# Kernel tuning notes

Hardware: AMD Instinct MI355X
Metric: run time of the kernel (lower is better)

## Reference

```python
import jax, jax.numpy as jnp
import numpy as np
from math import sqrt

N = 400000
MUL0, MUL1 = 64, 32            # multiplicities of 0e and 1o in irreps_in1 / irreps_out
DIM_IN1 = MUL0 + 3 * MUL1      # 160 = e3nn layout [64x0e | 32x1o]

# UnnormalisedFullyConnectedTensorProduct path coefficients:
# path_weight = mul1*mul2*n_paths_to_out, irrep_normalization='component',
# path_normalization='path' => coeff = sqrt(ir_out.dim / (mul1*mul2*n_paths_to_out)).
# Each output irrep (0e and 1o) receives exactly 2 paths here.
C_SS0 = sqrt(1.0 / (MUL0 * 1 * 2))   # 0e x 0e -> 0e
C_VV0 = sqrt(1.0 / (MUL1 * 1 * 2))   # 1o x 1o -> 0e
C_SV1 = sqrt(3.0 / (MUL0 * 1 * 2))   # 0e x 1o -> 1o
C_VS1 = sqrt(3.0 / (MUL1 * 1 * 2))   # 1o x 0e -> 1o
INV_SQRT3 = 1.0 / sqrt(3.0)          # real-basis wigner_3j values for the l=1 paths


def setup_inputs() -> dict:
    key = jax.random.key(0)
    ks = jax.random.split(key, 7)
    return {
        "x1": jax.random.normal(ks[0], (N, DIM_IN1), jnp.float32),
        "x2": jax.random.normal(ks[1], (N, 4), jnp.float32),   # 1x0e + 1x1o attribute
        # uvw weights, one [mul1, mul2, mul_out] block per CG path
        "W_ss0": jax.random.normal(ks[2], (MUL0, 1, MUL0), jnp.float32) * 0.05,
        "W_vv0": jax.random.normal(ks[3], (MUL1, 1, MUL0), jnp.float32) * 0.05,
        "W_sv1": jax.random.normal(ks[4], (MUL0, 1, MUL1), jnp.float32) * 0.05,
        "W_vs1": jax.random.normal(ks[5], (MUL1, 1, MUL1), jnp.float32) * 0.05,
        # bias only for the scalar (0e) output slice
        "bias0": jax.random.normal(ks[6], (MUL0,), jnp.float32) * 0.05,
    }


def reference(x1, x2, W_ss0, W_vv0, W_sv1, W_vs1, bias0):
    # split e3nn-layout inputs into irrep blocks
    s1 = x1[:, :MUL0]                      # [N, 64]     0e block
    v1 = x1[:, MUL0:].reshape(-1, MUL1, 3) # [N, 32, 3]  1o block (mul-major)
    s2 = x2[:, :1]                         # [N, 1]
    v2 = x2[:, 1:].reshape(-1, 1, 3)       # [N, 1, 3]

    # scalar output: 0e x 0e -> 0e  (w3j = [[[1]]])
    out0 = C_SS0 * jnp.einsum('uvw,bu,bv->bw', W_ss0, s1, s2)
    # scalar output: 1o x 1o -> 0e  (w3j[i,j,0] = delta_ij / sqrt(3))
    out0 = out0 + (C_VV0 * INV_SQRT3) * jnp.einsum('uvw,bui,bvi->bw', W_vv0, v1, v2)
    # slice-wise bias add on l=0 channels
    out0 = out0 + bias0

    # vector output: 0e x 1o -> 1o  (w3j[0,j,k] = delta_jk / sqrt(3))
    out1 = (C_SV1 * INV_SQRT3) * jnp.einsum('uvw,bu,bvk->bwk', W_sv1, s1, v2)
    # vector output: 1o x 0e -> 1o  (w3j[i,0,k] = delta_ik / sqrt(3))
    out1 = out1 + (C_VS1 * INV_SQRT3) * jnp.einsum('uvw,bui,bv->bwi', W_vs1, v1, s2)

    return jnp.concatenate([out0, out1.reshape(-1, MUL1 * 3)], axis=-1)  # [N, 160]
```

## Files before the change

kernel.cpp:

```cpp
#include <hip/hip_runtime.h>

typedef __bf16 bf16x8 __attribute__((ext_vector_type(8)));
typedef float floatx4 __attribute__((ext_vector_type(4)));

static constexpr int ROW_IN  = 160;
static constexpr int ROW_OUT = 160;

static constexpr float C_SS0_F    = 0.08838834764831845f;
static constexpr float C_VV0_I3_F = 0.07216878364870323f;
static constexpr float C_SV1_I3_F = 0.08838834764831845f;
static constexpr float C_VS1_I3_F = 0.125f;

__device__ __forceinline__ floatx4 mfma16(bf16x8 a, bf16x8 b, floatx4 c) {
    return __builtin_amdgcn_mfma_f32_16x16x32_bf16(a, b, c, 0, 0, 0);
}

__global__ __launch_bounds__(256, 2)
void o3tp_kernel(const float* __restrict__ x1, const float* __restrict__ x2,
                 const float* __restrict__ Wss0, const float* __restrict__ Wvv0,
                 const float* __restrict__ Wsv1, const float* __restrict__ Wvs1,
                 const float* __restrict__ bias0, float* __restrict__ out, int n)
{
    const int lane = threadIdx.x & 63;
    const int m = lane & 15;
    const int q = lane >> 4;

    bf16x8 Wss[2][4];
    bf16x8 Wvv[4];
    bf16x8 Wsv[2][2];
    bf16x8 Wvs[2];
#pragma unroll
    for (int kt = 0; kt < 2; ++kt)
#pragma unroll
        for (int ct = 0; ct < 4; ++ct)
#pragma unroll
            for (int j = 0; j < 8; ++j)
                Wss[kt][ct][j] = (__bf16)Wss0[(kt*32 + q*8 + j)*64 + ct*16 + m];
#pragma unroll
    for (int ct = 0; ct < 4; ++ct)
#pragma unroll
        for (int j = 0; j < 8; ++j)
            Wvv[ct][j] = (__bf16)Wvv0[(q*8 + j)*64 + ct*16 + m];
#pragma unroll
    for (int kt = 0; kt < 2; ++kt)
#pragma unroll
        for (int ct = 0; ct < 2; ++ct)
#pragma unroll
            for (int j = 0; j < 8; ++j)
                Wsv[kt][ct][j] = (__bf16)(Wsv1[(kt*32 + q*8 + j)*32 + ct*16 + m] * C_SV1_I3_F);
#pragma unroll
    for (int ct = 0; ct < 2; ++ct)
#pragma unroll
        for (int j = 0; j < 8; ++j)
            Wvs[ct][j] = (__bf16)Wvs1[(q*8 + j)*32 + ct*16 + m];

    floatx4 bias_v[4];
#pragma unroll
    for (int ct = 0; ct < 4; ++ct)
        bias_v[ct] = *(const floatx4*)(bias0 + ct*16 + q*4);

    const floatx4 zero = {0.f, 0.f, 0.f, 0.f};

    const int n_tiles = n >> 4;
    const int wid     = blockIdx.x * (blockDim.x >> 6) + (threadIdx.x >> 6);
    const int n_waves = gridDim.x * (blockDim.x >> 6);

    float4 rs[4];
    float4 rc[6];
    float4 rx2;

    auto LOAD = [&](int tile) {
        const float* __restrict__ src = x1 + (size_t)(tile*16 + m) * ROW_IN;
        rs[0] = *(const float4*)(src + q*8);
        rs[1] = *(const float4*)(src + q*8 + 4);
        rs[2] = *(const float4*)(src + 32 + q*8);
        rs[3] = *(const float4*)(src + 32 + q*8 + 4);
#pragma unroll
        for (int t = 0; t < 6; ++t)
            rc[t] = *(const float4*)(src + 64 + q*24 + t*4);
        rx2 = *(const float4*)(x2 + (size_t)(tile*16 + m) * 4);
    };

    int tile = wid;
    if (tile < n_tiles) LOAD(tile);

    for (; tile < n_tiles; ) {
        bf16x8 a_s[2], a_ss[2];
        const float sscale = rx2.x * C_SS0_F;
#pragma unroll
        for (int kt = 0; kt < 2; ++kt) {
            const float vv[8] = {rs[2*kt].x, rs[2*kt].y, rs[2*kt].z, rs[2*kt].w,
                                 rs[2*kt+1].x, rs[2*kt+1].y, rs[2*kt+1].z, rs[2*kt+1].w};
#pragma unroll
            for (int j = 0; j < 8; ++j) {
                a_s[kt][j]  = (__bf16)vv[j];
                a_ss[kt][j] = (__bf16)(vv[j] * sscale);
            }
        }
        float c[24];
#pragma unroll
        for (int t = 0; t < 6; ++t) {
            c[t*4+0] = rc[t].x; c[t*4+1] = rc[t].y; c[t*4+2] = rc[t].z; c[t*4+3] = rc[t].w;
        }
        bf16x8 a_d, a_v0, a_v1, a_v2;
        const float gscale = rx2.x * C_VS1_I3_F;
        const float xy = rx2.y, xz = rx2.z, xw = rx2.w;
#pragma unroll
        for (int j = 0; j < 8; ++j) {
            const float d = (c[3*j+0]*xy + c[3*j+1]*xz + c[3*j+2]*xw) * C_VV0_I3_F;
            a_d[j]  = (__bf16)d;
            a_v0[j] = (__bf16)(c[3*j+0] * gscale);
            a_v1[j] = (__bf16)(c[3*j+1] * gscale);
            a_v2[j] = (__bf16)(c[3*j+2] * gscale);
        }

        const int row0 = tile << 4;

        tile += n_waves;
        if (tile < n_tiles) LOAD(tile);

        floatx4 acc0[4], accT[2], accG0[2], accG1[2], accG2[2];
#pragma unroll
        for (int ct = 0; ct < 4; ++ct) {
            acc0[ct] = mfma16(Wss[0][ct], a_ss[0], zero);
            acc0[ct] = mfma16(Wss[1][ct], a_ss[1], acc0[ct]);
            acc0[ct] = mfma16(Wvv[ct],    a_d,     acc0[ct]);
        }
#pragma unroll
        for (int ct = 0; ct < 2; ++ct) {
            accT[ct]  = mfma16(Wsv[0][ct], a_s[0], zero);
            accT[ct]  = mfma16(Wsv[1][ct], a_s[1], accT[ct]);
            accG0[ct] = mfma16(Wvs[ct], a_v0, zero);
            accG1[ct] = mfma16(Wvs[ct], a_v1, zero);
            accG2[ct] = mfma16(Wvs[ct], a_v2, zero);
        }

        float* __restrict__ dst = out + (size_t)(row0 + m) * ROW_OUT;
#pragma unroll
        for (int ct = 0; ct < 4; ++ct) {
            floatx4 o;
#pragma unroll
            for (int r = 0; r < 4; ++r) o[r] = acc0[ct][r] + bias_v[ct][r];
            *(floatx4*)(dst + ct*16 + q*4) = o;
        }
#pragma unroll
        for (int ct = 0; ct < 2; ++ct) {
            float vals[12];
#pragma unroll
            for (int r = 0; r < 4; ++r) {
                const float t = accT[ct][r];
                vals[3*r+0] = fmaf(xy, t, accG0[ct][r]);
                vals[3*r+1] = fmaf(xz, t, accG1[ct][r]);
                vals[3*r+2] = fmaf(xw, t, accG2[ct][r]);
            }
            float* __restrict__ p = dst + 64 + 48*ct + 12*q;
#pragma unroll
            for (int s = 0; s < 3; ++s) {
                floatx4 o = {vals[4*s+0], vals[4*s+1], vals[4*s+2], vals[4*s+3]};
                *(floatx4*)(p + 4*s) = o;
            }
        }
    }
}

extern "C" void kernel_launch(void* const* d_in, const int* in_sizes, int n_in,
                              void* d_out, int out_size, void* d_ws, size_t ws_size,
                              hipStream_t stream) {
    const float* x1    = (const float*)d_in[0];
    const float* x2    = (const float*)d_in[1];
    const float* Wss0  = (const float*)d_in[2];
    const float* Wvv0  = (const float*)d_in[3];
    const float* Wsv1  = (const float*)d_in[4];
    const float* Wvs1  = (const float*)d_in[5];
    const float* bias0 = (const float*)d_in[6];
    float* out = (float*)d_out;
    const int n = in_sizes[0] / ROW_IN;

    dim3 grid(512), block(256);
    hipLaunchKernelGGL(o3tp_kernel, grid, block, 0, stream,
                       x1, x2, Wss0, Wvv0, Wsv1, Wvs1, bias0, out, n);
}
```

Baseline: 453.5 us.

## Stage x1 tiles through LDS with coalesced global loads; fold bias into MFMA accumulator

Each wave now loads its 16x160 x1 tile with fully coalesced contiguous float4 loads, writes it into a padded per-wave LDS buffer, and reads back the per-lane scattered fragments from LDS. This replaces the strided per-row global loads, which touched many cache lines per instruction. The bias is now used as the initial MFMA accumulator instead of a separate add. The change costs LDS traffic, an extra lgkmcnt wait, and a strided LDS write that may bank-conflict.

```diff
diff --git a/kernel.cpp b/kernel.cpp
--- a/kernel.cpp
+++ b/kernel.cpp
@@ -5,6 +5,7 @@
 
 static constexpr int ROW_IN  = 160;
 static constexpr int ROW_OUT = 160;
+static constexpr int LDS_STRIDE = 164;
 
 static constexpr float C_SS0_F    = 0.08838834764831845f;
 static constexpr float C_VV0_I3_F = 0.07216878364870323f;
@@ -21,6 +22,9 @@
                  const float* __restrict__ Wsv1, const float* __restrict__ Wvs1,
                  const float* __restrict__ bias0, float* __restrict__ out, int n)
 {
+    __shared__ float lds[4][16 * LDS_STRIDE];
+    float* __restrict__ tl = lds[threadIdx.x >> 6];
+
     const int lane = threadIdx.x & 63;
     const int m = lane & 15;
     const int q = lane >> 4;
@@ -54,10 +58,10 @@
         for (int j = 0; j < 8; ++j)
             Wvs[ct][j] = (__bf16)Wvs1[(q*8 + j)*32 + ct*16 + m];
 
-    floatx4 bias_v[4];
+    floatx4 bias_c[4];
 #pragma unroll
     for (int ct = 0; ct < 4; ++ct)
-        bias_v[ct] = *(const floatx4*)(bias0 + ct*16 + q*4);
+        bias_c[ct] = *(const floatx4*)(bias0 + ct*16 + q*4);
 
     const floatx4 zero = {0.f, 0.f, 0.f, 0.f};
 
@@ -65,46 +69,71 @@
     const int wid     = blockIdx.x * (blockDim.x >> 6) + (threadIdx.x >> 6);
     const int n_waves = gridDim.x * (blockDim.x >> 6);
 
-    float4 rs[4];
-    float4 rc[6];
+    float4 v[10];
     float4 rx2;
 
-    auto LOAD = [&](int tile) {
-        const float* __restrict__ src = x1 + (size_t)(tile*16 + m) * ROW_IN;
-        rs[0] = *(const float4*)(src + q*8);
-        rs[1] = *(const float4*)(src + q*8 + 4);
-        rs[2] = *(const float4*)(src + 32 + q*8);
-        rs[3] = *(const float4*)(src + 32 + q*8 + 4);
+    auto GLOAD = [&](int t) {
+        const float* __restrict__ src = x1 + (size_t)(t << 4) * ROW_IN;
+#pragma unroll
+        for (int it = 0; it < 10; ++it)
+            v[it] = *(const float4*)(src + (it*64 + lane)*4);
+        rx2 = *(const float4*)(x2 + (size_t)((t << 4) + m) * 4);
+    };
+    auto LDSWRITE = [&]() {
+#pragma unroll
+        for (int it = 0; it < 10; ++it) {
+            const int f   = it*64 + lane;
+            const int row = f / 40;
+            const int col = f*4 - row*ROW_IN;
+            *(float4*)(tl + row*LDS_STRIDE + col) = v[it];
+        }
+    };
+
+    int tile = wid;
+    if (tile >= n_tiles) return;
+
+    GLOAD(tile);
+    LDSWRITE();
+    asm volatile("s_waitcnt lgkmcnt(0)" ::: "memory");
+
+    for (; tile < n_tiles; ) {
+        const float sx = rx2.x, xy = rx2.y, xz = rx2.z, xw = rx2.w;
+        const int row0 = tile << 4;
+
+        tile += n_waves;
+        const bool have_next = (tile < n_tiles);
+        if (have_next) GLOAD(tile);
+
+        const float* __restrict__ xr = tl + m * LDS_STRIDE;
+        float4 s0 = *(const float4*)(xr + q*8);
+        float4 s1 = *(const float4*)(xr + q*8 + 4);
+        float4 s2 = *(const float4*)(xr + 32 + q*8);
+        float4 s3 = *(const float4*)(xr + 32 + q*8 + 4);
+        float4 cc[6];
 #pragma unroll
         for (int t = 0; t < 6; ++t)
-            rc[t] = *(const float4*)(src + 64 + q*24 + t*4);
-        rx2 = *(const float4*)(x2 + (size_t)(tile*16 + m) * 4);
-    };
-
-    int tile = wid;
-    if (tile < n_tiles) LOAD(tile);
-
-    for (; tile < n_tiles; ) {
+            cc[t] = *(const float4*)(xr + 64 + q*24 + t*4);
+
         bf16x8 a_s[2], a_ss[2];
-        const float sscale = rx2.x * C_SS0_F;
-#pragma unroll
-        for (int kt = 0; kt < 2; ++kt) {
-            const float vv[8] = {rs[2*kt].x, rs[2*kt].y, rs[2*kt].z, rs[2*kt].w,
-                                 rs[2*kt+1].x, rs[2*kt+1].y, rs[2*kt+1].z, rs[2*kt+1].w};
+        const float sscale = sx * C_SS0_F;
+        {
+            const float vv0[8] = {s0.x, s0.y, s0.z, s0.w, s1.x, s1.y, s1.z, s1.w};
+            const float vv1[8] = {s2.x, s2.y, s2.z, s2.w, s3.x, s3.y, s3.z, s3.w};
 #pragma unroll
             for (int j = 0; j < 8; ++j) {
-                a_s[kt][j]  = (__bf16)vv[j];
-                a_ss[kt][j] = (__bf16)(vv[j] * sscale);
+                a_s[0][j]  = (__bf16)vv0[j];
+                a_ss[0][j] = (__bf16)(vv0[j] * sscale);
+                a_s[1][j]  = (__bf16)vv1[j];
+                a_ss[1][j] = (__bf16)(vv1[j] * sscale);
             }
         }
         float c[24];
 #pragma unroll
         for (int t = 0; t < 6; ++t) {
-            c[t*4+0] = rc[t].x; c[t*4+1] = rc[t].y; c[t*4+2] = rc[t].z; c[t*4+3] = rc[t].w;
+            c[t*4+0] = cc[t].x; c[t*4+1] = cc[t].y; c[t*4+2] = cc[t].z; c[t*4+3] = cc[t].w;
         }
         bf16x8 a_d, a_v0, a_v1, a_v2;
-        const float gscale = rx2.x * C_VS1_I3_F;
-        const float xy = rx2.y, xz = rx2.z, xw = rx2.w;
+        const float gscale = sx * C_VS1_I3_F;
 #pragma unroll
         for (int j = 0; j < 8; ++j) {
             const float d = (c[3*j+0]*xy + c[3*j+1]*xz + c[3*j+2]*xw) * C_VV0_I3_F;
@@ -114,15 +143,10 @@
             a_v2[j] = (__bf16)(c[3*j+2] * gscale);
         }
 
-        const int row0 = tile << 4;
-
-        tile += n_waves;
-        if (tile < n_tiles) LOAD(tile);
-
         floatx4 acc0[4], accT[2], accG0[2], accG1[2], accG2[2];
 #pragma unroll
         for (int ct = 0; ct < 4; ++ct) {
-            acc0[ct] = mfma16(Wss[0][ct], a_ss[0], zero);
+            acc0[ct] = mfma16(Wss[0][ct], a_ss[0], bias_c[ct]);
             acc0[ct] = mfma16(Wss[1][ct], a_ss[1], acc0[ct]);
             acc0[ct] = mfma16(Wvv[ct],    a_d,     acc0[ct]);
         }
@@ -137,12 +161,8 @@
 
         float* __restrict__ dst = out + (size_t)(row0 + m) * ROW_OUT;
 #pragma unroll
-        for (int ct = 0; ct < 4; ++ct) {
-            floatx4 o;
-#pragma unroll
-            for (int r = 0; r < 4; ++r) o[r] = acc0[ct][r] + bias_v[ct][r];
-            *(floatx4*)(dst + ct*16 + q*4) = o;
-        }
+        for (int ct = 0; ct < 4; ++ct)
+            *(floatx4*)(dst + ct*16 + q*4) = acc0[ct];
 #pragma unroll
         for (int ct = 0; ct < 2; ++ct) {
             float vals[12];
@@ -159,6 +179,12 @@
                 floatx4 o = {vals[4*s+0], vals[4*s+1], vals[4*s+2], vals[4*s+3]};
                 *(floatx4*)(p + 4*s) = o;
             }
+        }
+
+        if (have_next) {
+            asm volatile("" ::: "memory");
+            LDSWRITE();
+            asm volatile("s_waitcnt lgkmcnt(0)" ::: "memory");
         }
     }
 }
```

Result: slower. 500.2 us (+10.3%).
